# Performance work log

Measured on AMD Instinct MI355X. Metric: run time of the kernel, lower is better.

## Reference

```python
import jax, jax.numpy as jnp
import numpy as np

B, S, F_IN, F_OUT = 8, 128, 768, 768
NUM_REL = 41           # num_dependencies + 1
NUM_LAYER = 2
N_HEAD, HID = 8, 96    # hidden_dim = embed_dim // n_head
EMB = 768


def setup_inputs() -> dict:
    key = jax.random.key(0)
    ks = jax.random.split(key, 14)
    s = 1.0 / np.sqrt(F_IN)
    inp = {
        "x": jax.random.normal(ks[0], (B, S, F_IN), dtype=jnp.float32),
        "adj": jax.random.uniform(ks[1], (B, NUM_REL, S, S), dtype=jnp.float32),
        "q": jax.random.normal(ks[2], (B, EMB), dtype=jnp.float32),
        # R-GCN params (stacked over layers)
        "w_rgcn": jax.random.uniform(ks[3], (NUM_LAYER, NUM_REL, F_IN, F_OUT), minval=-s, maxval=s),
        "score_w": jax.random.uniform(ks[4], (NUM_LAYER, F_OUT), minval=-s, maxval=s),
        "score_b": jax.random.uniform(ks[5], (NUM_LAYER,), minval=-s, maxval=s),
        # Attention params (stored as [in, out] for x @ W)
        "wk": jax.random.uniform(ks[6], (EMB, N_HEAD * HID), minval=-s, maxval=s),
        "bk": jnp.zeros((N_HEAD * HID,), jnp.float32),
        "wq": jax.random.uniform(ks[7], (EMB, N_HEAD * HID), minval=-s, maxval=s),
        "bq": jnp.zeros((N_HEAD * HID,), jnp.float32),
        "wbil": jax.random.uniform(ks[8], (HID, HID), minval=-1.0 / np.sqrt(HID), maxval=1.0 / np.sqrt(HID)),
        "wproj": jax.random.uniform(ks[9], (N_HEAD * HID, EMB), minval=-s, maxval=s),
        "bproj": jnp.zeros((EMB,), jnp.float32),
    }
    return inp


def _rgcn_layer(h, adj, w, sw, sb):
    # h: [B,S,I]; adj: [B,R,S,S]; w: [R,I,O]
    hidden = jnp.einsum("bsi,rio->brso", h, w)            # per-relation transform
    denom = jnp.sum(adj, axis=3, keepdims=True)           # [B,R,S,1]
    intm = jnp.einsum("brsk,brko->brso", adj, hidden)     # relation-wise aggregation
    div = intm / jnp.where(denom == 0, jnp.ones_like(denom), denom)
    logits = jnp.einsum("brso,o->brs", div, sw) + sb      # score Linear(out->1)
    r_coeffs = jax.nn.softmax(logits, axis=1)             # softmax over relations
    out = jnp.einsum("brso,brs->bso", div, r_coeffs)
    return jax.nn.relu(out)


def _attention(k, q, wk, bk, wq, bq, wbil, wproj, bproj):
    # k: [B,S,E]; q: [B,E] -> [B,1,E]
    q3 = q[:, None, :]
    kx = (k @ wk + bk).reshape(B, S, N_HEAD, HID)
    qx = (q3 @ wq + bq).reshape(B, 1, N_HEAD, HID)
    qw = jnp.einsum("bqhd,de->bqhe", qx, wbil)            # bi_linear score
    score = jnp.einsum("bqhe,bkhe->bhqk", qw, kx)
    attn = jax.nn.softmax(score, axis=-1)
    o = jnp.einsum("bhqk,bkhd->bqhd", attn, kx).reshape(B, 1, N_HEAD * HID)
    return o @ wproj + bproj                              # [B,1,EMB]


def reference(x, adj, q, w_rgcn, score_w, score_b, wk, bk, wq, bq, wbil, wproj, bproj):
    h = x
    for l in range(NUM_LAYER):
        h = _rgcn_layer(h, adj, w_rgcn[l], score_w[l], score_b[l])
    return _attention(h, q, wk, bk, wq, bq, wbil, wproj, bproj)
```

## Files before the change

kernel.cpp:

```cpp
#include <hip/hip_runtime.h>
#include <stdint.h>

#define B_ 8
#define S_ 128
#define R_ 41
#define F_ 768
#define NH_ 8
#define HID_ 96
#define BS_ (B_*S_)
#define SM_SCALE 256.0f

typedef _Float16 f16;
typedef _Float16 f16x8 __attribute__((ext_vector_type(8)));
typedef _Float16 f16x4 __attribute__((ext_vector_type(4)));
typedef float f32x4 __attribute__((ext_vector_type(4)));

#define GLD16(gp, lp) __builtin_amdgcn_global_load_lds((const __attribute__((address_space(1))) uint32_t*)(gp), (__attribute__((address_space(3))) uint32_t*)(lp), 16, 0, 0)

__device__ __forceinline__ float wredsum(float v){
  #pragma unroll
  for (int o=32;o;o>>=1) v += __shfl_down(v,o,64);
  return v;
}

__global__ __launch_bounds__(256) void kConvW(const float* __restrict__ w, f16* __restrict__ wT) {
  int bid = blockIdx.x;
  int ot = bid % 12; int it = (bid/12) % 12; int r = bid / 144;
  __shared__ float t[64*68];
  int tid = threadIdx.x;
  int ri = tid >> 2, c = tid & 3;
  const float* src = w + ((size_t)r*F_ + (it*64 + ri))*F_ + ot*64 + c*16;
  #pragma unroll
  for (int j=0;j<4;j++){
    f32x4 v4 = *(const f32x4*)(src + j*4);
    *(f32x4*)&t[ri*68 + c*16 + j*4] = v4;
  }
  __syncthreads();
  int ro = tid >> 2;
  f16 outv[16];
  #pragma unroll
  for (int j=0;j<16;j++) outv[j] = (f16)t[(c*16+j)*68 + ro];
  f16* dst = wT + ((size_t)r*F_ + (ot*64+ro))*F_ + it*64 + c*16;
  *(f16x8*)dst = *(f16x8*)&outv[0];
  *(f16x8*)(dst+8) = *(f16x8*)&outv[8];
}

__global__ __launch_bounds__(256) void kV(const float* __restrict__ w, const float* __restrict__ sw, float* __restrict__ v) {
  int idx = blockIdx.x*4 + (threadIdx.x>>6);
  int lane = threadIdx.x & 63;
  const float* row = w + (size_t)idx*F_ + lane*12;
  const float* swp = sw + lane*12;
  float acc = 0.f;
  #pragma unroll
  for (int j=0;j<3;j++){
    f32x4 a = *(const f32x4*)(row + j*4);
    f32x4 b = *(const f32x4*)(swp + j*4);
    acc += a.x*b.x + a.y*b.y + a.z*b.z + a.w*b.w;
  }
  acc = wredsum(acc);
  if (lane==0) v[idx] = acc;
}

template<typename T>
__global__ __launch_bounds__(256) void kTransTo16T(const T* __restrict__ h, f16* __restrict__ hT) {
  int bid = blockIdx.x;
  int st = bid & 1; int ft = (bid>>1) % 12; int b = bid / 24;
  __shared__ f16 t[64*72];
  int tid = threadIdx.x;
  int sl = tid>>2, c = tid&3;
  const T* src = h + ((size_t)b*S_ + st*64 + sl)*F_ + ft*64 + c*16;
  f16 tmp[16];
  #pragma unroll
  for (int j=0;j<16;j++) tmp[j] = (f16)src[j];
  *(f16x8*)&t[sl*72 + c*16]     = *(f16x8*)&tmp[0];
  *(f16x8*)&t[sl*72 + c*16 + 8] = *(f16x8*)&tmp[8];
  __syncthreads();
  int fl = tid>>2;
  f16 outv[16];
  #pragma unroll
  for (int j=0;j<16;j++) outv[j] = t[(c*16+j)*72 + fl];
  f16* dst = hT + ((size_t)b*F_ + ft*64 + fl)*S_ + st*64 + c*16;
  *(f16x8*)dst = *(f16x8*)&outv[0];
  *(f16x8*)(dst+8) = *(f16x8*)&outv[8];
}

__global__ __launch_bounds__(256) void kU(const float* __restrict__ h, const float* __restrict__ v, float* __restrict__ u) {
  int idx = blockIdx.x*4 + (threadIdx.x>>6);
  int lane = threadIdx.x&63;
  int k = idx & 127;
  int br = idx >> 7;
  int r = br % R_;
  int b = br / R_;
  const float* hr = h + ((size_t)b*S_ + k)*F_ + lane*12;
  const float* vr = v + (size_t)r*F_ + lane*12;
  float acc=0.f;
  #pragma unroll
  for (int j=0;j<3;j++){
    f32x4 a = *(const f32x4*)(hr+j*4);
    f32x4 c4 = *(const f32x4*)(vr+j*4);
    acc += a.x*c4.x+a.y*c4.y+a.z*c4.z+a.w*c4.w;
  }
  acc = wredsum(acc);
  if (lane==0) u[idx] = acc;
}

__global__ __launch_bounds__(256) void kLogits(const float* __restrict__ adj, const float* __restrict__ u,
                        const float* __restrict__ sb_all, int l,
                        float* __restrict__ dinv, float* __restrict__ lg) {
  int idx = blockIdx.x*4 + (threadIdx.x>>6);
  int lane = threadIdx.x&63;
  const float* arow = adj + (size_t)idx*S_;
  int br = idx >> 7;
  const float* up = u + (size_t)br*S_;
  float a0 = arow[lane], a1 = arow[lane+64];
  float u0 = up[lane],   u1 = up[lane+64];
  float ssum = a0+a1;
  float sdot = a0*u0 + a1*u1;
  ssum = wredsum(ssum);
  sdot = wredsum(sdot);
  if (lane==0){
    float dv = (ssum==0.0f) ? 1.0f : (1.0f/ssum);
    dinv[idx] = dv;
    lg[idx] = sdot*dv + sb_all[l];
  }
}

__global__ __launch_bounds__(256) void kSoftmaxR(const float* __restrict__ lg, float* __restrict__ c) {
  int t = blockIdx.x*256 + threadIdx.x;
  int b = t >> 7, s = t & 127;
  float vals[R_];
  float mx = -1e30f;
  #pragma unroll
  for (int r=0;r<R_;r++){ float x = lg[((size_t)b*R_+r)*S_ + s]; vals[r]=x; mx = fmaxf(mx,x); }
  float sum=0.f;
  #pragma unroll
  for (int r=0;r<R_;r++){ vals[r] = expf(vals[r]-mx); sum += vals[r]; }
  float inv = 1.0f/sum;
  #pragma unroll
  for (int r=0;r<R_;r++) c[((size_t)b*R_+r)*S_+s] = vals[r]*inv;
}

__global__ __launch_bounds__(256) void kM16(const float* __restrict__ adj, const float* __restrict__ c,
                     const float* __restrict__ dinv, f16* __restrict__ M) {
  int t = blockIdx.x*256 + threadIdx.x;
  int brs = t >> 5; int k4 = (t & 31) * 4;
  float a = SM_SCALE * c[brs] * dinv[brs];
  f32x4 v4 = *(const f32x4*)(adj + (size_t)brs*S_ + k4);
  f16x4 o;
  o[0]=(f16)(v4.x*a); o[1]=(f16)(v4.y*a); o[2]=(f16)(v4.z*a); o[3]=(f16)(v4.w*a);
  *(f16x4*)(M + (size_t)brs*S_ + k4) = o;
}

__global__ __launch_bounds__(256) void kGgemm(const f16* __restrict__ M, const f16* __restrict__ hT, f16* __restrict__ G) {
  __shared__ f16 lds[128*128 + 64*128];
  f16* lsA = lds;
  f16* lsB = lds + 16384;
  int bid = blockIdx.x;
  int nt = bid % 12; int r = (bid/12) % R_; int b = bid/(12*R_);
  int tid = threadIdx.x, wid = tid>>6, lane = tid&63;
  const f16* Ab = M + (size_t)(b*R_ + r)*(S_*S_);
  const f16* Bb = hT + ((size_t)b*F_ + nt*64)*S_;
  #pragma unroll
  for (int j=0;j<8;j++){
    int qd = wid*8 + j;
    GLD16(Ab + qd*512 + lane*8, lsA + qd*512);
  }
  #pragma unroll
  for (int j=0;j<4;j++){
    int qd = wid*4 + j;
    GLD16(Bb + qd*512 + lane*8, lsB + qd*512);
  }
  __syncthreads();
  f32x4 acc[4][2] = {};
  int wr = wid>>1, wc = wid&1;
  int lr = lane&15, kk0 = (lane>>4)*8;
  #pragma unroll
  for (int ks=0;ks<4;ks++){
    int kk = ks*32 + kk0;
    f16x8 av[4], bv[2];
    #pragma unroll
    for (int i=0;i<4;i++) av[i] = *(const f16x8*)&lsA[(wr*64+i*16+lr)*128 + kk];
    #pragma unroll
    for (int i=0;i<2;i++) bv[i] = *(const f16x8*)&lsB[(wc*32+i*16+lr)*128 + kk];
    #pragma unroll
    for (int mi=0;mi<4;mi++)
      #pragma unroll
      for (int ni=0;ni<2;ni++)
        acc[mi][ni] = __builtin_amdgcn_mfma_f32_16x16x32_f16(av[mi],bv[ni],acc[mi][ni],0,0,0);
  }
  __syncthreads();
  #pragma unroll
  for (int mi=0;mi<4;mi++)
    #pragma unroll
    for (int ni=0;ni<2;ni++){
      int row = wr*64 + mi*16 + (lane>>4)*4;
      int col = wc*32 + ni*16 + lr;
      #pragma unroll
      for (int i=0;i<4;i++)
        lds[(row+i)*80 + col] = (f16)acc[mi][ni][i];
    }
  __syncthreads();
  int row = tid>>1, seg = tid&1;
  f16* dst = G + ((size_t)(b*R_ + r)*S_ + row)*F_ + nt*64 + seg*32;
  const f16* sl = lds + row*80 + seg*32;
  #pragma unroll
  for (int j=0;j<4;j++) *(f16x8*)(dst + j*8) = *(const f16x8*)(sl + j*8);
}

__global__ __launch_bounds__(256) void kOutGemm(const f16* __restrict__ G, const f16* __restrict__ WT, float* __restrict__ Cp) {
  __shared__ f16 lsA[128*64];
  __shared__ f16 lsB[128*64];
  int bid = blockIdx.x;
  int g = bid % 12, nt = (bid/12) % 6, mt = bid/72;
  int r0 = (g<5)? g*4 : 20 + (g-5)*3;
  int nr = (g<5)? 4 : 3;
  int tid = threadIdx.x, wid = tid>>6, lane = tid&63;
  size_t abase[4], bbase[4];
  #pragma unroll
  for (int j=0;j<4;j++){
    int qd = wid*4 + j;
    int row = mt*128 + qd*8 + (lane>>3);
    int b = row >> 7, s = row & 127;
    abase[j] = ((size_t)b*R_*S_ + s)*F_ + (lane&7)*8;
    int o = nt*128 + qd*8 + (lane>>3);
    bbase[j] = (size_t)o*F_ + (lane&7)*8;
  }
  f32x4 acc[4][4] = {};
  int wr = wid>>1, wc = wid&1;
  int lr = lane&15, kk0 = (lane>>4)*8;
  for (int rr=0; rr<nr; ++rr){
    int r = r0 + rr;
    const f16* Ar = G  + (size_t)r*S_*F_;
    const f16* Br = WT + (size_t)r*F_*F_;
    for (int it=0; it<12; ++it){
      #pragma unroll
      for (int j=0;j<4;j++){
        int qd = wid*4+j;
        GLD16(Ar + abase[j] + it*64, lsA + qd*512);
        GLD16(Br + bbase[j] + it*64, lsB + qd*512);
      }
      __syncthreads();
      #pragma unroll
      for (int ks=0;ks<2;ks++){
        int kk = ks*32 + kk0;
        f16x8 av[4], bv[4];
        #pragma unroll
        for (int i=0;i<4;i++) av[i] = *(const f16x8*)&lsA[(wr*64+i*16+lr)*64 + kk];
        #pragma unroll
        for (int i=0;i<4;i++) bv[i] = *(const f16x8*)&lsB[(wc*64+i*16+lr)*64 + kk];
        #pragma unroll
        for (int mi=0;mi<4;mi++)
          #pragma unroll
          for (int ni=0;ni<4;ni++)
            acc[mi][ni] = __builtin_amdgcn_mfma_f32_16x16x32_f16(av[mi],bv[ni],acc[mi][ni],0,0,0);
      }
      __syncthreads();
    }
  }
  #pragma unroll
  for (int mi=0;mi<4;mi++)
    #pragma unroll
    for (int ni=0;ni<4;ni++){
      int row = mt*128 + wr*64 + mi*16 + (lane>>4)*4;
      int col = nt*128 + wc*64 + ni*16 + lr;
      #pragma unroll
      for (int i=0;i<4;i++)
        Cp[((size_t)g*BS_ + row + i)*F_ + col] = acc[mi][ni][i];
    }
}

__global__ __launch_bounds__(256) void kReduce(const float* __restrict__ Cp, float* __restrict__ h32, f16* __restrict__ h16o) {
  int t = blockIdx.x*256 + threadIdx.x;
  size_t i4 = (size_t)t*4;
  f32x4 s = {};
  #pragma unroll
  for (int g=0; g<12; g++){
    f32x4 v4 = *(const f32x4*)(Cp + (size_t)g*BS_*F_ + i4);
    s.x += v4.x; s.y += v4.y; s.z += v4.z; s.w += v4.w;
  }
  const float inv = 1.0f/SM_SCALE;
  f32x4 rr;
  rr.x = fmaxf(s.x*inv, 0.f); rr.y = fmaxf(s.y*inv, 0.f);
  rr.z = fmaxf(s.z*inv, 0.f); rr.w = fmaxf(s.w*inv, 0.f);
  *(f32x4*)(h32 + i4) = rr;
  f16x4 o; o[0]=(f16)rr.x; o[1]=(f16)rr.y; o[2]=(f16)rr.z; o[3]=(f16)rr.w;
  *(f16x4*)(h16o + i4) = o;
}

__global__ __launch_bounds__(256) void kKx(const f16* __restrict__ A, const f16* __restrict__ BT,
                    const float* __restrict__ bias, float* __restrict__ C) {
  __shared__ f16 lsA[128*64];
  __shared__ f16 lsB[128*64];
  int bid = blockIdx.x;
  int nt = bid % 6, mt = bid / 6;
  int tid = threadIdx.x, wid = tid>>6, lane = tid&63;
  size_t abase[4], bbase[4];
  #pragma unroll
  for (int j=0;j<4;j++){
    int qd = wid*4 + j;
    int row = mt*128 + qd*8 + (lane>>3);
    abase[j] = (size_t)row*F_ + (lane&7)*8;
    int o = nt*128 + qd*8 + (lane>>3);
    bbase[j] = (size_t)o*F_ + (lane&7)*8;
  }
  f32x4 acc[4][4] = {};
  int wr = wid>>1, wc = wid&1;
  int lr = lane&15, kk0 = (lane>>4)*8;
  for (int it=0; it<12; ++it){
    #pragma unroll
    for (int j=0;j<4;j++){
      int qd = wid*4+j;
      GLD16(A + abase[j] + it*64, lsA + qd*512);
      GLD16(BT + bbase[j] + it*64, lsB + qd*512);
    }
    __syncthreads();
    #pragma unroll
    for (int ks=0;ks<2;ks++){
      int kk = ks*32 + kk0;
      f16x8 av[4], bv[4];
      #pragma unroll
      for (int i=0;i<4;i++) av[i] = *(const f16x8*)&lsA[(wr*64+i*16+lr)*64 + kk];
      #pragma unroll
      for (int i=0;i<4;i++) bv[i] = *(const f16x8*)&lsB[(wc*64+i*16+lr)*64 + kk];
      #pragma unroll
      for (int mi=0;mi<4;mi++)
        #pragma unroll
        for (int ni=0;ni<4;ni++)
          acc[mi][ni] = __builtin_amdgcn_mfma_f32_16x16x32_f16(av[mi],bv[ni],acc[mi][ni],0,0,0);
    }
    __syncthreads();
  }
  #pragma unroll
  for (int mi=0;mi<4;mi++)
    #pragma unroll
    for (int ni=0;ni<4;ni++){
      int row = mt*128 + wr*64 + mi*16 + (lane>>4)*4;
      int col = nt*128 + wc*64 + ni*16 + lr;
      float bb = bias[col];
      #pragma unroll
      for (int i=0;i<4;i++)
        C[(size_t)(row+i)*F_ + col] = acc[mi][ni][i] + bb;
    }
}

__global__ __launch_bounds__(256) void kAttn(const float* __restrict__ kx, const float* __restrict__ qin,
                      const float* __restrict__ wq, const float* __restrict__ bq,
                      const float* __restrict__ wbil, float* __restrict__ obuf) {
  int bid = blockIdx.x; int h = bid & 7; int b = bid >> 3;
  __shared__ float qx[HID_], qw[HID_], sc[S_];
  __shared__ float smax, ssum;
  int t = threadIdx.x;
  if (t < HID_) {
    float acc=0.f;
    const float* qp = qin + (size_t)b*F_;
    const float* wp = wq + h*HID_ + t;
    for (int i=0;i<F_;i++) acc += qp[i]*wp[(size_t)i*F_];
    qx[t] = acc + bq[h*HID_+t];
  }
  __syncthreads();
  if (t < HID_) {
    float acc=0.f;
    for (int e=0;e<HID_;e++) acc += qx[e]*wbil[e*HID_+t];
    qw[t] = acc;
  }
  __syncthreads();
  if (t < S_) {
    float acc=0.f;
    const float* kp = kx + ((size_t)b*S_ + t)*F_ + h*HID_;
    for (int e=0;e<HID_;e++) acc += qw[e]*kp[e];
    sc[t] = acc;
  }
  __syncthreads();
  if (t==0){ float m=-1e30f; for(int k=0;k<S_;k++) m=fmaxf(m,sc[k]); smax=m; }
  __syncthreads();
  if (t < S_) sc[t] = expf(sc[t]-smax);
  __syncthreads();
  if (t==0){ float s=0.f; for(int k=0;k<S_;k++) s+=sc[k]; ssum=s; }
  __syncthreads();
  if (t < HID_) {
    float acc=0.f;
    const float* kp = kx + ((size_t)b*S_)*F_ + h*HID_ + t;
    for (int k=0;k<S_;k++) acc += sc[k]*kp[(size_t)k*F_];
    obuf[(size_t)b*F_ + h*HID_ + t] = acc/ssum;
  }
}

__global__ __launch_bounds__(256) void kProj(const float* __restrict__ obuf, const float* __restrict__ wproj,
                      const float* __restrict__ bproj, float* __restrict__ outp) {
  int b = blockIdx.x; int t = threadIdx.x;
  __shared__ float ov[F_];
  for (int j=t;j<F_;j+=256) ov[j] = obuf[(size_t)b*F_ + j];
  __syncthreads();
  float a0=bproj[t], a1=bproj[t+256], a2=bproj[t+512];
  for (int j=0;j<F_;j++){
    float o_ = ov[j];
    const float* wr_ = wproj + (size_t)j*F_;
    a0 += o_*wr_[t]; a1 += o_*wr_[t+256]; a2 += o_*wr_[t+512];
  }
  outp[(size_t)b*F_ + t]       = a0;
  outp[(size_t)b*F_ + t + 256] = a1;
  outp[(size_t)b*F_ + t + 512] = a2;
}

extern "C" void kernel_launch(void* const* d_in, const int* in_sizes, int n_in,
                              void* d_out, int out_size, void* d_ws, size_t ws_size,
                              hipStream_t stream) {
  (void)in_sizes; (void)n_in; (void)out_size;
  const float* x      = (const float*)d_in[0];
  const float* adj    = (const float*)d_in[1];
  const float* qin    = (const float*)d_in[2];
  const float* w_rgcn = (const float*)d_in[3];
  const float* score_w= (const float*)d_in[4];
  const float* score_b= (const float*)d_in[5];
  const float* wk     = (const float*)d_in[6];
  const float* bk     = (const float*)d_in[7];
  const float* wq     = (const float*)d_in[8];
  const float* bq     = (const float*)d_in[9];
  const float* wbil   = (const float*)d_in[10];
  const float* wproj  = (const float*)d_in[11];
  const float* bproj  = (const float*)d_in[12];
  float* outp = (float*)d_out;

  char* p = (char*)d_ws;
  auto alloc = [&](size_t bytes)->char* {
    char* r = p; p += (bytes + 255) & ~(size_t)255; return r;
  };
  f16*   w16T  = (f16*)  alloc((size_t)R_*F_*F_*2);
  f16*   G16   = (f16*)  alloc((size_t)B_*R_*S_*F_*2);
  f16*   M16   = (f16*)  alloc((size_t)B_*R_*S_*S_*2);
  float* Cpart = (float*)alloc((size_t)12*BS_*F_*4);
  float* h32a  = (float*)alloc((size_t)BS_*F_*4);
  float* h32b  = (float*)alloc((size_t)BS_*F_*4);
  f16*   h16row= (f16*)  alloc((size_t)BS_*F_*2);
  f16*   h16T  = (f16*)  alloc((size_t)BS_*F_*2);
  float* kx    = (float*)alloc((size_t)BS_*F_*4);
  f16*   wkT   = (f16*)  alloc((size_t)F_*F_*2);
  float* vbuf  = (float*)alloc((size_t)R_*F_*4);
  float* ubuf  = (float*)alloc((size_t)B_*R_*S_*4);
  float* dinv  = (float*)alloc((size_t)B_*R_*S_*4);
  float* lgb   = (float*)alloc((size_t)B_*R_*S_*4);
  float* cbuf  = (float*)alloc((size_t)B_*R_*S_*4);
  float* obuf  = (float*)alloc((size_t)B_*F_*4);
  if ((size_t)(p - (char*)d_ws) > ws_size) return;

  const size_t WL = (size_t)R_*F_*F_;

  kConvW<<<R_*144, 256, 0, stream>>>(w_rgcn, w16T);
  kV<<<7872, 256, 0, stream>>>(w_rgcn, score_w, vbuf);
  kTransTo16T<float><<<192, 256, 0, stream>>>(x, h16T);
  kU<<<10496, 256, 0, stream>>>(x, vbuf, ubuf);
  kLogits<<<10496, 256, 0, stream>>>(adj, ubuf, score_b, 0, dinv, lgb);
  kSoftmaxR<<<4, 256, 0, stream>>>(lgb, cbuf);
  kM16<<<5248, 256, 0, stream>>>(adj, cbuf, dinv, M16);
  kGgemm<<<B_*R_*12, 256, 0, stream>>>(M16, h16T, G16);
  kOutGemm<<<576, 256, 0, stream>>>(G16, w16T, Cpart);
  kReduce<<<768, 256, 0, stream>>>(Cpart, h32a, h16row);
  kTransTo16T<f16><<<192, 256, 0, stream>>>(h16row, h16T);

  kConvW<<<R_*144, 256, 0, stream>>>(w_rgcn + WL, w16T);
  kV<<<7872, 256, 0, stream>>>(w_rgcn + WL, score_w + F_, vbuf);
  kU<<<10496, 256, 0, stream>>>(h32a, vbuf, ubuf);
  kLogits<<<10496, 256, 0, stream>>>(adj, ubuf, score_b, 1, dinv, lgb);
  kSoftmaxR<<<4, 256, 0, stream>>>(lgb, cbuf);
  kM16<<<5248, 256, 0, stream>>>(adj, cbuf, dinv, M16);
  kGgemm<<<B_*R_*12, 256, 0, stream>>>(M16, h16T, G16);
  kOutGemm<<<576, 256, 0, stream>>>(G16, w16T, Cpart);
  kReduce<<<768, 256, 0, stream>>>(Cpart, h32b, h16row);

  kConvW<<<144, 256, 0, stream>>>(wk, wkT);
  kKx<<<48, 256, 0, stream>>>(h16row, wkT, bk, kx);
  kAttn<<<64, 256, 0, stream>>>(kx, qin, wq, bq, wbil, obuf);
  kProj<<<8, 256, 0, stream>>>(obuf, wproj, bproj, outp);
}
```

Measured before the change: 574.7 us.

## Fuse weight conversion with score-vector dot, widen Ggemm tile, tune attention and projection

Merges the fp16 weight transpose and the per-row score-vector dot product into one kernel, so the 41x768x768 fp32 weight tensor is read once per layer instead of twice. Doubles the N tile of the relation-aggregation GEMM to 128 columns, halving how often the adjacency tile is reloaded at the cost of fewer blocks and more registers and LDS per block. Reorders the output-GEMM block index so blocks sharing an A tile run close together. Adds multiple accumulators and wave-shuffle reductions in attention, and splits the projection across more blocks to raise parallelism.

```diff
diff --git a/kernel.cpp b/kernel.cpp
--- a/kernel.cpp
+++ b/kernel.cpp
@@ -23,6 +23,39 @@
   return v;
 }
 
+__global__ __launch_bounds__(256) void kConvWV(const float* __restrict__ w, const float* __restrict__ sw,
+                                               f16* __restrict__ wT, float* __restrict__ v) {
+  int bid = blockIdx.x;
+  int it = bid % 12, r = bid / 12;
+  __shared__ float t[64*68];
+  int tid = threadIdx.x;
+  int ri = tid >> 2, c = tid & 3;
+  float vacc = 0.f;
+  for (int ot = 0; ot < 12; ++ot) {
+    const float* src = w + ((size_t)r*F_ + (it*64 + ri))*F_ + ot*64 + c*16;
+    const float* swp = sw + ot*64 + c*16;
+    __syncthreads();
+    #pragma unroll
+    for (int j=0;j<4;j++){
+      f32x4 v4 = *(const f32x4*)(src + j*4);
+      f32x4 s4 = *(const f32x4*)(swp + j*4);
+      vacc += v4.x*s4.x + v4.y*s4.y + v4.z*s4.z + v4.w*s4.w;
+      *(f32x4*)&t[ri*68 + c*16 + j*4] = v4;
+    }
+    __syncthreads();
+    int ro = tid >> 2;
+    f16 outv[16];
+    #pragma unroll
+    for (int j=0;j<16;j++) outv[j] = (f16)t[(c*16+j)*68 + ro];
+    f16* dst = wT + ((size_t)r*F_ + (ot*64+ro))*F_ + it*64 + c*16;
+    *(f16x8*)dst = *(f16x8*)&outv[0];
+    *(f16x8*)(dst+8) = *(f16x8*)&outv[8];
+  }
+  vacc += __shfl_down(vacc, 1, 64);
+  vacc += __shfl_down(vacc, 2, 64);
+  if (c == 0) v[(size_t)r*F_ + it*64 + ri] = vacc;
+}
+
 __global__ __launch_bounds__(256) void kConvW(const float* __restrict__ w, f16* __restrict__ wT) {
   int bid = blockIdx.x;
   int ot = bid % 12; int it = (bid/12) % 12; int r = bid / 144;
@@ -43,22 +76,6 @@
   f16* dst = wT + ((size_t)r*F_ + (ot*64+ro))*F_ + it*64 + c*16;
   *(f16x8*)dst = *(f16x8*)&outv[0];
   *(f16x8*)(dst+8) = *(f16x8*)&outv[8];
-}
-
-__global__ __launch_bounds__(256) void kV(const float* __restrict__ w, const float* __restrict__ sw, float* __restrict__ v) {
-  int idx = blockIdx.x*4 + (threadIdx.x>>6);
-  int lane = threadIdx.x & 63;
-  const float* row = w + (size_t)idx*F_ + lane*12;
-  const float* swp = sw + lane*12;
-  float acc = 0.f;
-  #pragma unroll
-  for (int j=0;j<3;j++){
-    f32x4 a = *(const f32x4*)(row + j*4);
-    f32x4 b = *(const f32x4*)(swp + j*4);
-    acc += a.x*b.x + a.y*b.y + a.z*b.z + a.w*b.w;
-  }
-  acc = wredsum(acc);
-  if (lane==0) v[idx] = acc;
 }
 
 template<typename T>
@@ -152,66 +169,62 @@
 }
 
 __global__ __launch_bounds__(256) void kGgemm(const f16* __restrict__ M, const f16* __restrict__ hT, f16* __restrict__ G) {
-  __shared__ f16 lds[128*128 + 64*128];
+  __shared__ f16 lds[2*16384];
   f16* lsA = lds;
   f16* lsB = lds + 16384;
   int bid = blockIdx.x;
-  int nt = bid % 12; int r = (bid/12) % R_; int b = bid/(12*R_);
+  int nt = bid % 6; int r = (bid/6) % R_; int b = bid/(6*R_);
   int tid = threadIdx.x, wid = tid>>6, lane = tid&63;
   const f16* Ab = M + (size_t)(b*R_ + r)*(S_*S_);
-  const f16* Bb = hT + ((size_t)b*F_ + nt*64)*S_;
+  const f16* Bb = hT + ((size_t)b*F_ + nt*128)*S_;
   #pragma unroll
   for (int j=0;j<8;j++){
     int qd = wid*8 + j;
     GLD16(Ab + qd*512 + lane*8, lsA + qd*512);
-  }
-  #pragma unroll
-  for (int j=0;j<4;j++){
-    int qd = wid*4 + j;
     GLD16(Bb + qd*512 + lane*8, lsB + qd*512);
   }
   __syncthreads();
-  f32x4 acc[4][2] = {};
+  f32x4 acc[4][4] = {};
   int wr = wid>>1, wc = wid&1;
   int lr = lane&15, kk0 = (lane>>4)*8;
   #pragma unroll
   for (int ks=0;ks<4;ks++){
     int kk = ks*32 + kk0;
-    f16x8 av[4], bv[2];
+    f16x8 av[4], bv[4];
     #pragma unroll
     for (int i=0;i<4;i++) av[i] = *(const f16x8*)&lsA[(wr*64+i*16+lr)*128 + kk];
     #pragma unroll
-    for (int i=0;i<2;i++) bv[i] = *(const f16x8*)&lsB[(wc*32+i*16+lr)*128 + kk];
+    for (int i=0;i<4;i++) bv[i] = *(const f16x8*)&lsB[(wc*64+i*16+lr)*128 + kk];
     #pragma unroll
     for (int mi=0;mi<4;mi++)
       #pragma unroll
-      for (int ni=0;ni<2;ni++)
+      for (int ni=0;ni<4;ni++)
         acc[mi][ni] = __builtin_amdgcn_mfma_f32_16x16x32_f16(av[mi],bv[ni],acc[mi][ni],0,0,0);
   }
   __syncthreads();
   #pragma unroll
   for (int mi=0;mi<4;mi++)
     #pragma unroll
-    for (int ni=0;ni<2;ni++){
+    for (int ni=0;ni<4;ni++){
       int row = wr*64 + mi*16 + (lane>>4)*4;
-      int col = wc*32 + ni*16 + lr;
+      int col = wc*64 + ni*16 + lr;
       #pragma unroll
       for (int i=0;i<4;i++)
-        lds[(row+i)*80 + col] = (f16)acc[mi][ni][i];
+        lds[(row+i)*136 + col] = (f16)acc[mi][ni][i];
     }
   __syncthreads();
   int row = tid>>1, seg = tid&1;
-  f16* dst = G + ((size_t)(b*R_ + r)*S_ + row)*F_ + nt*64 + seg*32;
-  const f16* sl = lds + row*80 + seg*32;
-  #pragma unroll
-  for (int j=0;j<4;j++) *(f16x8*)(dst + j*8) = *(const f16x8*)(sl + j*8);
+  f16* dst = G + ((size_t)(b*R_ + r)*S_ + row)*F_ + nt*128 + seg*64;
+  const f16* sl = lds + row*136 + seg*64;
+  #pragma unroll
+  for (int j=0;j<8;j++) *(f16x8*)(dst + j*8) = *(const f16x8*)(sl + j*8);
 }
 
 __global__ __launch_bounds__(256) void kOutGemm(const f16* __restrict__ G, const f16* __restrict__ WT, float* __restrict__ Cp) {
   __shared__ f16 lsA[128*64];
   __shared__ f16 lsB[128*64];
   int bid = blockIdx.x;
-  int g = bid % 12, nt = (bid/12) % 6, mt = bid/72;
+  int nt = bid % 6, g = (bid/6) % 12, mt = bid/72;
   int r0 = (g<5)? g*4 : 20 + (g-5)*3;
   int nr = (g<5)? 4 : 3;
   int tid = threadIdx.x, wid = tid>>6, lane = tid&63;
@@ -351,55 +364,70 @@
   __shared__ float smax, ssum;
   int t = threadIdx.x;
   if (t < HID_) {
-    float acc=0.f;
+    float a0=0.f,a1=0.f,a2=0.f,a3=0.f;
     const float* qp = qin + (size_t)b*F_;
     const float* wp = wq + h*HID_ + t;
-    for (int i=0;i<F_;i++) acc += qp[i]*wp[(size_t)i*F_];
-    qx[t] = acc + bq[h*HID_+t];
+    for (int i=0;i<F_;i+=4){
+      a0 += qp[i]*wp[(size_t)i*F_];
+      a1 += qp[i+1]*wp[(size_t)(i+1)*F_];
+      a2 += qp[i+2]*wp[(size_t)(i+2)*F_];
+      a3 += qp[i+3]*wp[(size_t)(i+3)*F_];
+    }
+    qx[t] = a0+a1+a2+a3 + bq[h*HID_+t];
   }
   __syncthreads();
   if (t < HID_) {
-    float acc=0.f;
-    for (int e=0;e<HID_;e++) acc += qx[e]*wbil[e*HID_+t];
-    qw[t] = acc;
+    float a0=0.f,a1=0.f;
+    for (int e=0;e<HID_;e+=2){ a0 += qx[e]*wbil[e*HID_+t]; a1 += qx[e+1]*wbil[(e+1)*HID_+t]; }
+    qw[t] = a0+a1;
   }
   __syncthreads();
   if (t < S_) {
-    float acc=0.f;
+    float a0=0.f,a1=0.f;
     const float* kp = kx + ((size_t)b*S_ + t)*F_ + h*HID_;
-    for (int e=0;e<HID_;e++) acc += qw[e]*kp[e];
-    sc[t] = acc;
-  }
-  __syncthreads();
-  if (t==0){ float m=-1e30f; for(int k=0;k<S_;k++) m=fmaxf(m,sc[k]); smax=m; }
+    for (int e=0;e<HID_;e+=2){ a0 += qw[e]*kp[e]; a1 += qw[e+1]*kp[e+1]; }
+    sc[t] = a0+a1;
+  }
+  __syncthreads();
+  if (t < 64) {
+    float m = fmaxf(sc[t], sc[t+64]);
+    #pragma unroll
+    for (int o=32;o;o>>=1) m = fmaxf(m, __shfl_down(m,o,64));
+    if (t==0) smax = m;
+  }
   __syncthreads();
   if (t < S_) sc[t] = expf(sc[t]-smax);
   __syncthreads();
-  if (t==0){ float s=0.f; for(int k=0;k<S_;k++) s+=sc[k]; ssum=s; }
+  if (t < 64) {
+    float s = sc[t] + sc[t+64];
+    s = wredsum(s);
+    if (t==0) ssum = s;
+  }
   __syncthreads();
   if (t < HID_) {
-    float acc=0.f;
+    float a0=0.f,a1=0.f;
     const float* kp = kx + ((size_t)b*S_)*F_ + h*HID_ + t;
-    for (int k=0;k<S_;k++) acc += sc[k]*kp[(size_t)k*F_];
-    obuf[(size_t)b*F_ + h*HID_ + t] = acc/ssum;
+    for (int k=0;k<S_;k+=2){ a0 += sc[k]*kp[(size_t)k*F_]; a1 += sc[k+1]*kp[(size_t)(k+1)*F_]; }
+    obuf[(size_t)b*F_ + h*HID_ + t] = (a0+a1)/ssum;
   }
 }
 
 __global__ __launch_bounds__(256) void kProj(const float* __restrict__ obuf, const float* __restrict__ wproj,
                       const float* __restrict__ bproj, float* __restrict__ outp) {
-  int b = blockIdx.x; int t = threadIdx.x;
+  int bid = blockIdx.x; int b = bid/3, seg = bid%3;
+  int t = threadIdx.x;
   __shared__ float ov[F_];
   for (int j=t;j<F_;j+=256) ov[j] = obuf[(size_t)b*F_ + j];
   __syncthreads();
-  float a0=bproj[t], a1=bproj[t+256], a2=bproj[t+512];
-  for (int j=0;j<F_;j++){
-    float o_ = ov[j];
-    const float* wr_ = wproj + (size_t)j*F_;
-    a0 += o_*wr_[t]; a1 += o_*wr_[t+256]; a2 += o_*wr_[t+512];
-  }
-  outp[(size_t)b*F_ + t]       = a0;
-  outp[(size_t)b*F_ + t + 256] = a1;
-  outp[(size_t)b*F_ + t + 512] = a2;
+  int col = seg*256 + t;
+  float a0=0.f,a1=0.f,a2=0.f,a3=0.f;
+  for (int j=0;j<F_;j+=4){
+    a0 += ov[j]*wproj[(size_t)j*F_+col];
+    a1 += ov[j+1]*wproj[(size_t)(j+1)*F_+col];
+    a2 += ov[j+2]*wproj[(size_t)(j+2)*F_+col];
+    a3 += ov[j+3]*wproj[(size_t)(j+3)*F_+col];
+  }
+  outp[(size_t)b*F_ + col] = bproj[col] + a0+a1+a2+a3;
 }
 
 extern "C" void kernel_launch(void* const* d_in, const int* in_sizes, int n_in,
@@ -445,30 +473,28 @@
 
   const size_t WL = (size_t)R_*F_*F_;
 
-  kConvW<<<R_*144, 256, 0, stream>>>(w_rgcn, w16T);
-  kV<<<7872, 256, 0, stream>>>(w_rgcn, score_w, vbuf);
+  kConvWV<<<R_*12, 256, 0, stream>>>(w_rgcn, score_w, w16T, vbuf);
   kTransTo16T<float><<<192, 256, 0, stream>>>(x, h16T);
   kU<<<10496, 256, 0, stream>>>(x, vbuf, ubuf);
   kLogits<<<10496, 256, 0, stream>>>(adj, ubuf, score_b, 0, dinv, lgb);
   kSoftmaxR<<<4, 256, 0, stream>>>(lgb, cbuf);
   kM16<<<5248, 256, 0, stream>>>(adj, cbuf, dinv, M16);
-  kGgemm<<<B_*R_*12, 256, 0, stream>>>(M16, h16T, G16);
+  kGgemm<<<B_*R_*6, 256, 0, stream>>>(M16, h16T, G16);
   kOutGemm<<<576, 256, 0, stream>>>(G16, w16T, Cpart);
   kReduce<<<768, 256, 0, stream>>>(Cpart, h32a, h16row);
   kTransTo16T<f16><<<192, 256, 0, stream>>>(h16row, h16T);
 
-  kConvW<<<R_*144, 256, 0, stream>>>(w_rgcn + WL, w16T);
-  kV<<<7872, 256, 0, stream>>>(w_rgcn + WL, score_w + F_, vbuf);
+  kConvWV<<<R_*12, 256, 0, stream>>>(w_rgcn + WL, score_w + F_, w16T, vbuf);
   kU<<<10496, 256, 0, stream>>>(h32a, vbuf, ubuf);
   kLogits<<<10496, 256, 0, stream>>>(adj, ubuf, score_b, 1, dinv, lgb);
   kSoftmaxR<<<4, 256, 0, stream>>>(lgb, cbuf);
   kM16<<<5248, 256, 0, stream>>>(adj, cbuf, dinv, M16);
-  kGgemm<<<B_*R_*12, 256, 0, stream>>>(M16, h16T, G16);
+  kGgemm<<<B_*R_*6, 256, 0, stream>>>(M16, h16T, G16);
   kOutGemm<<<576, 256, 0, stream>>>(G16, w16T, Cpart);
   kReduce<<<768, 256, 0, stream>>>(Cpart, h32b, h16row);
 
   kConvW<<<144, 256, 0, stream>>>(wk, wkT);
   kKx<<<48, 256, 0, stream>>>(h16row, wkT, bk, kx);
   kAttn<<<64, 256, 0, stream>>>(kx, qin, wq, bq, wbil, obuf);
-  kProj<<<8, 256, 0, stream>>>(obuf, wproj, bproj, outp);
-}
+  kProj<<<24, 256, 0, stream>>>(obuf, wproj, bproj, outp);
+}
```

Result: faster. 530.4 us (-7.7%).
